# Optimization experiments

Hardware: AMD Instinct MI355X
Metric: run time of the kernel (lower is better)

## Reference

```python
import jax, jax.numpy as jnp
import numpy as np

B, C, H, W = 4, 256, 48, 48
HEADS, DIM_HEAD, SCALE = 8, 64, 10.0
INNER = HEADS * DIM_HEAD
EPS = 1e-12


def setup_inputs() -> dict:
    key = jax.random.key(0)
    k1, k2, k3, k4 = jax.random.split(key, 4)
    x = jax.random.normal(k1, (B, C, H, W), dtype=jnp.float32)
    # 1x1 conv weights stored as [out_ch, in_ch]
    w_qkv = jax.random.normal(k2, (3 * INNER, C), dtype=jnp.float32) * (1.0 / np.sqrt(C))
    w_out = jax.random.normal(k3, (C, INNER), dtype=jnp.float32) * (1.0 / np.sqrt(INNER))
    b_out = jax.random.normal(k4, (C,), dtype=jnp.float32) * 0.01
    return {"x": x, "w_qkv": w_qkv, "w_out": w_out, "b_out": b_out}


def _l2norm(t):
    # normalize along last axis, clamping the norm at EPS (matches torch l2norm)
    denom = jnp.maximum(jnp.linalg.norm(t, axis=-1, keepdims=True), EPS)
    return t / denom


def reference(x, w_qkv, w_out, b_out):
    b, c, h, w = x.shape
    n = h * w
    # 1x1 conv QKV projection: [B, 3*INNER, H, W]
    qkv = jnp.einsum('oc,bchw->bohw', w_qkv, x)
    q, k, v = jnp.split(qkv, 3, axis=1)
    # [B, heads, dim_head, N] -> [B, heads, N, dim_head]
    def to_bhnd(t):
        return t.reshape(b, HEADS, DIM_HEAD, n).transpose(0, 1, 3, 2)
    q = _l2norm(to_bhnd(q))
    k = _l2norm(to_bhnd(k))
    v = to_bhnd(v)
    sim = jnp.einsum('bhid,bhjd->bhij', q, k) * SCALE  # [B,h,N,N]
    attn = jax.nn.softmax(sim, axis=-1)
    out = jnp.einsum('bhij,bhjd->bhid', attn, v)  # [B,h,N,d]
    # back to [B, INNER, H, W]
    out = out.transpose(0, 1, 3, 2).reshape(b, INNER, h, w)
    # 1x1 conv output projection with bias
    out = jnp.einsum('oc,bchw->bohw', w_out, out) + b_out[None, :, None, None]
    return out
```

## Files before the change

### kernel.cpp

```cpp
#include <hip/hip_runtime.h>

typedef unsigned short u16;
typedef __attribute__((ext_vector_type(8))) short bf16x8;
typedef __attribute__((ext_vector_type(4))) float f32x4;
typedef __attribute__((ext_vector_type(16))) float f32x16;

#define MFMA16(A,B,C) __builtin_amdgcn_mfma_f32_16x16x32_bf16(A,B,C,0,0,0)
#define MFMA32(A,B,C) __builtin_amdgcn_mfma_f32_32x32x16_bf16(A,B,C,0,0,0)

#define B_ 4
#define C_ 256
#define N_ 2304
#define HEADS_ 8
#define DH_ 64
#define INNER_ 512
#define SCALE_LOG2E 14.426950408889634f

__device__ __forceinline__ u16 f2bf(float f) {
    union { float f; unsigned int u; } v; v.f = f;
    unsigned int r = v.u + 0x7fffu + ((v.u >> 16) & 1u);
    return (u16)(r >> 16);
}
__device__ __forceinline__ float bf2f(u16 h) {
    union { unsigned int u; float f; } v; v.u = ((unsigned int)h) << 16;
    return v.f;
}
__device__ __forceinline__ unsigned int cvtpk(float a, float b) {
    unsigned int r;
    asm("v_cvt_pk_bf16_f32 %0, %1, %2" : "=v"(r) : "v"(a), "v"(b));
    return r;
}
__device__ __forceinline__ void pl32swap(unsigned &a, unsigned &b) {
    asm volatile("v_permlane32_swap_b32 %0, %1" : "+v"(a), "+v"(b));
}
__device__ __forceinline__ float fexp2(float x) {
    float r;
    asm("v_exp_f32 %0, %1" : "=v"(r) : "v"(x));
    return r;
}

__global__ __launch_bounds__(256) void k_prep(const float* __restrict__ x,
                                              u16* __restrict__ xT,
                                              const float* __restrict__ w_qkv,
                                              u16* __restrict__ wqb,
                                              const float* __restrict__ w_out,
                                              u16* __restrict__ wob) {
    __shared__ float tile[64][65];
    int idx = blockIdx.x;
    int t = threadIdx.x;
    if (idx < 576) {
        int b = idx / 144, rem = idx % 144;
        int n0 = (rem >> 2) * 64, c0 = (rem & 3) * 64;
        const float* xb = x + (size_t)b * C_ * N_;
        u16* xTb = xT + (size_t)b * N_ * C_;
        int r = t >> 4;
        int q4 = (t & 15) * 4;
#pragma unroll
        for (int pass = 0; pass < 4; ++pass) {
            int c = r + pass * 16;
            float4 v = *(const float4*)(xb + (size_t)(c0 + c) * N_ + n0 + q4);
            tile[c][q4+0] = v.x; tile[c][q4+1] = v.y; tile[c][q4+2] = v.z; tile[c][q4+3] = v.w;
        }
        __syncthreads();
#pragma unroll
        for (int pass = 0; pass < 4; ++pass) {
            int n = r + pass * 16;
            ushort4 o;
            o.x = f2bf(tile[q4+0][n]); o.y = f2bf(tile[q4+1][n]);
            o.z = f2bf(tile[q4+2][n]); o.w = f2bf(tile[q4+3][n]);
            *(ushort4*)(xTb + (size_t)(n0 + n) * C_ + c0 + q4) = o;
        }
    } else if (idx < 960) {
        int i = (idx - 576) * 256 + t;
        float4 v = ((const float4*)w_qkv)[i];
        ushort4 o;
        o.x = f2bf(v.x); o.y = f2bf(v.y); o.z = f2bf(v.z); o.w = f2bf(v.w);
        ((ushort4*)wqb)[i] = o;
    } else {
        int i = (idx - 960) * 256 + t;
        float4 v = ((const float4*)w_out)[i];
        ushort4 o;
        o.x = f2bf(v.x); o.y = f2bf(v.y); o.z = f2bf(v.z); o.w = f2bf(v.w);
        ((ushort4*)wob)[i] = o;
    }
}

__global__ __launch_bounds__(256) void k_qkv(const u16* __restrict__ w_qkv,
                                             const u16* __restrict__ xT,
                                             u16* __restrict__ Qn,
                                             u16* __restrict__ Kn,
                                             u16* __restrict__ Vt) {
    __shared__ __align__(16) u16 Wt[64][264];
    __shared__ __align__(16) u16 Xt[64][264];
    int mt = blockIdx.x, nt = blockIdx.y, b = blockIdx.z;
    int tid = threadIdx.x;
    int wv = tid >> 6, lane = tid & 63;
    int col = lane & 15, quad = lane >> 4;
    int o0 = mt * 64;
    const u16* wtile = w_qkv + (size_t)o0 * C_;
    const u16* xtile = xT + ((size_t)b * N_ + nt*64) * C_;
#pragma unroll
    for (int p = 0; p < 8; ++p) {
        int c = p * 256 + tid;
        int row = c >> 5, seg = c & 31;
        *(uint4*)(&Wt[row][seg*8]) = *(const uint4*)(wtile + (size_t)row * C_ + seg*8);
        *(uint4*)(&Xt[row][seg*8]) = *(const uint4*)(xtile + (size_t)row * C_ + seg*8);
    }
    __syncthreads();
    f32x4 z = {0.f, 0.f, 0.f, 0.f};
    f32x4 acc[4]; acc[0]=z; acc[1]=z; acc[2]=z; acc[3]=z;
#pragma unroll
    for (int ks = 0; ks < 8; ++ks) {
        bf16x8 bfrag = *(const bf16x8*)(&Xt[wv*16 + col][ks*32 + quad*8]);
#pragma unroll
        for (int mb = 0; mb < 4; ++mb) {
            bf16x8 afrag = *(const bf16x8*)(&Wt[mb*16 + col][ks*32 + quad*8]);
            acc[mb] = MFMA16(afrag, bfrag, acc[mb]);
        }
    }
    int n = nt * 64 + wv * 16 + col;
    int which = mt >> 3, h = mt & 7;
    if (which < 2) {
        float s = 0.f;
#pragma unroll
        for (int mb = 0; mb < 4; ++mb)
#pragma unroll
            for (int r = 0; r < 4; ++r) s += acc[mb][r] * acc[mb][r];
        s += __shfl_xor(s, 16);
        s += __shfl_xor(s, 32);
        float inv = 1.f / fmaxf(sqrtf(s), 1e-12f);
        if (which == 0) inv *= SCALE_LOG2E;
        u16* dst = (which == 0 ? Qn : Kn) + (((size_t)b * HEADS_ + h) * N_ + n) * DH_;
#pragma unroll
        for (int mb = 0; mb < 4; ++mb) {
            uint2 o;
            o.x = cvtpk(acc[mb][0] * inv, acc[mb][1] * inv);
            o.y = cvtpk(acc[mb][2] * inv, acc[mb][3] * inv);
            *(uint2*)(dst + mb*16 + quad*4) = o;
        }
    } else {
        u16* dst = Vt + ((size_t)b * HEADS_ + h) * (size_t)DH_ * N_;
#pragma unroll
        for (int mb = 0; mb < 4; ++mb)
#pragma unroll
            for (int r = 0; r < 4; ++r)
                dst[(size_t)(mb*16 + quad*4 + r) * N_ + n] = f2bf(acc[mb][r]);
    }
}

__device__ __forceinline__ void store_o32(const f32x16 O, u16* dst, int hi) {
    unsigned c0 = cvtpk(O[0], O[1]),  c1 = cvtpk(O[2], O[3]);
    unsigned c2 = cvtpk(O[4], O[5]),  c3 = cvtpk(O[6], O[7]);
    unsigned c4 = cvtpk(O[8], O[9]),  c5 = cvtpk(O[10], O[11]);
    unsigned c6 = cvtpk(O[12], O[13]), c7 = cvtpk(O[14], O[15]);
    pl32swap(c0, c2); pl32swap(c1, c3);
    pl32swap(c4, c6); pl32swap(c5, c7);
    uint4 w0; w0.x = c0; w0.y = c1; w0.z = c2; w0.w = c3;
    uint4 w1; w1.x = c4; w1.y = c5; w1.z = c6; w1.w = c7;
    *(uint4*)(dst + hi*8)      = w0;
    *(uint4*)(dst + 16 + hi*8) = w1;
}

#define SM_PACK(S, PF0, PF1, LSUM)                                              \
    {                                                                           \
        _Pragma("unroll")                                                       \
        for (int i = 0; i < 16; ++i) S[i] = fexp2(S[i]);                        \
        LSUM += ( ((S[0]+S[1])+(S[2]+S[3])) + ((S[4]+S[5])+(S[6]+S[7])) )       \
              + ( ((S[8]+S[9])+(S[10]+S[11])) + ((S[12]+S[13])+(S[14]+S[15])) );\
        unsigned c0 = cvtpk(S[0], S[1]),  c1 = cvtpk(S[2], S[3]);               \
        unsigned c2 = cvtpk(S[4], S[5]),  c3 = cvtpk(S[6], S[7]);               \
        unsigned c4 = cvtpk(S[8], S[9]),  c5 = cvtpk(S[10], S[11]);             \
        unsigned c6 = cvtpk(S[12], S[13]), c7 = cvtpk(S[14], S[15]);            \
        pl32swap(c0, c2); pl32swap(c1, c3);                                     \
        pl32swap(c4, c6); pl32swap(c5, c7);                                     \
        PF0.u[0] = c0; PF0.u[1] = c1; PF0.u[2] = c2; PF0.u[3] = c3;             \
        PF1.u[0] = c4; PF1.u[1] = c5; PF1.u[2] = c6; PF1.u[3] = c7;             \
    }

__global__ __launch_bounds__(256) void k_attn_split(const u16* __restrict__ Qn,
                                                    const u16* __restrict__ Kn,
                                                    const u16* __restrict__ Vt,
                                                    u16* __restrict__ Opb,
                                                    float* __restrict__ lp) {
    __shared__ __align__(16) u16 Kt[2][64][72];
    __shared__ __align__(16) u16 Vtl[2][64][72];
    int head_lin = blockIdx.x & 31;
    int rest = blockIdx.x >> 5;
    int qt = rest % 18;
    int ksplit = rest / 18;
    int b = head_lin >> 3, h = head_lin & 7;
    int tid = threadIdx.x;
    int wv = tid >> 6, lane = tid & 63;
    int q32 = lane & 31, hi = lane >> 5;
    size_t head = (size_t)b * HEADS_ + h;
    const u16* Qh = Qn + head * (size_t)N_ * DH_;
    const u16* Kh = Kn + head * (size_t)N_ * DH_ + (size_t)ksplit * 576 * DH_;
    const u16* Vh = Vt + head * (size_t)DH_ * N_;
    int q0 = qt * 128 + wv * 32;
    bf16x8 qf[4];
#pragma unroll
    for (int ds = 0; ds < 4; ++ds)
        qf[ds] = *(const bf16x8*)(Qh + (size_t)(q0 + q32) * DH_ + ds*16 + hi*8);
    f32x16 accO0, accO1;
#pragma unroll
    for (int i = 0; i < 16; ++i) { accO0[i] = 0.f; accO1[i] = 0.f; }
    float lsum = 0.f;
    int srow = tid >> 3, sseg = tid & 7;
    const u16* ksrc0 = Kh + (size_t)tid * 8;
    const u16* vsrc0 = Vh + (size_t)srow * N_ + ksplit * 576 + sseg * 8;

    uint4 k0 = *(const uint4*)(ksrc0);
    uint4 k1 = *(const uint4*)(ksrc0 + 2048);
    uint4 v0 = *(const uint4*)(vsrc0);
    uint4 v1 = *(const uint4*)(vsrc0 + (size_t)32 * N_);
    *(uint4*)(&Kt[0][srow][sseg*8])       = k0;
    *(uint4*)(&Kt[0][32 + srow][sseg*8])  = k1;
    *(uint4*)(&Vtl[0][srow][sseg*8])      = v0;
    *(uint4*)(&Vtl[0][32 + srow][sseg*8]) = v1;
    int cur = 0;

    for (int kt = 0; kt < 9; ++kt) {
        __syncthreads();
        int ktn = kt + 1 < 9 ? kt + 1 : kt;
        k0 = *(const uint4*)(ksrc0 + (size_t)ktn * 4096);
        k1 = *(const uint4*)(ksrc0 + (size_t)ktn * 4096 + 2048);
        v0 = *(const uint4*)(vsrc0 + ktn * 64);
        v1 = *(const uint4*)(vsrc0 + (size_t)32 * N_ + ktn * 64);
        const u16 (*Ktc)[72]  = Kt[cur];
        const u16 (*Vtc)[72]  = Vtl[cur];
        f32x16 s0, s1;
#pragma unroll
        for (int i = 0; i < 16; ++i) { s0[i] = 0.f; s1[i] = 0.f; }
        __builtin_amdgcn_s_setprio(1);
#pragma unroll
        for (int ds = 0; ds < 4; ++ds) {
            bf16x8 kf = *(const bf16x8*)(&Ktc[q32][ds*16 + hi*8]);
            s0 = MFMA32(kf, qf[ds], s0);
        }
#pragma unroll
        for (int ds = 0; ds < 4; ++ds) {
            bf16x8 kf = *(const bf16x8*)(&Ktc[32 + q32][ds*16 + hi*8]);
            s1 = MFMA32(kf, qf[ds], s1);
        }
        __builtin_amdgcn_s_setprio(0);
        union { unsigned u[4]; bf16x8 v; } pfA, pfB, pfC, pfD;
        SM_PACK(s0, pfA, pfB, lsum)
        __builtin_amdgcn_s_setprio(1);
        {
            bf16x8 vf00 = *(const bf16x8*)(&Vtc[q32][hi*8]);
            bf16x8 vf01 = *(const bf16x8*)(&Vtc[32 + q32][hi*8]);
            accO0 = MFMA32(vf00, pfA.v, accO0);
            accO1 = MFMA32(vf01, pfA.v, accO1);
            bf16x8 vf10 = *(const bf16x8*)(&Vtc[q32][16 + hi*8]);
            bf16x8 vf11 = *(const bf16x8*)(&Vtc[32 + q32][16 + hi*8]);
            accO0 = MFMA32(vf10, pfB.v, accO0);
            accO1 = MFMA32(vf11, pfB.v, accO1);
        }
        __builtin_amdgcn_s_setprio(0);
        SM_PACK(s1, pfC, pfD, lsum)
        __builtin_amdgcn_s_setprio(1);
        {
            bf16x8 vf00 = *(const bf16x8*)(&Vtc[q32][32 + hi*8]);
            bf16x8 vf01 = *(const bf16x8*)(&Vtc[32 + q32][32 + hi*8]);
            accO0 = MFMA32(vf00, pfC.v, accO0);
            accO1 = MFMA32(vf01, pfC.v, accO1);
            bf16x8 vf10 = *(const bf16x8*)(&Vtc[q32][48 + hi*8]);
            bf16x8 vf11 = *(const bf16x8*)(&Vtc[32 + q32][48 + hi*8]);
            accO0 = MFMA32(vf10, pfD.v, accO0);
            accO1 = MFMA32(vf11, pfD.v, accO1);
        }
        __builtin_amdgcn_s_setprio(0);
        {
            u16 (*Ktn_)[72] = Kt[cur ^ 1];
            u16 (*Vtn_)[72] = Vtl[cur ^ 1];
            *(uint4*)(&Ktn_[srow][sseg*8])      = k0;
            *(uint4*)(&Ktn_[32 + srow][sseg*8]) = k1;
            *(uint4*)(&Vtn_[srow][sseg*8])      = v0;
            *(uint4*)(&Vtn_[32 + srow][sseg*8]) = v1;
        }
        cur ^= 1;
    }
    lsum += __shfl_xor(lsum, 32);
    u16* dst = Opb + (((size_t)ksplit * B_ + b) * N_ + q0 + q32) * INNER_ + h * DH_;
    store_o32(accO0, dst, hi);
    store_o32(accO1, dst + 32, hi);
    if (hi == 0) {
        size_t lbase = (((size_t)ksplit * B_ + b) * HEADS_ + h) * N_;
        lp[lbase + q0 + q32] = lsum;
    }
}

__global__ __launch_bounds__(256) void k_comb(const u16* __restrict__ Opb,
                                              const float* __restrict__ lp,
                                              u16* __restrict__ AO) {
    int g = blockIdx.x * 256 + threadIdx.x;
    int b = g / 294912;
    int rem = g % 294912;
    int n = rem >> 7;
    int i4 = rem & 127;
    int h = i4 >> 4;
    float s0 = 0.f, s1 = 0.f, s2 = 0.f, s3 = 0.f, l = 0.f;
#pragma unroll
    for (int s = 0; s < 4; ++s) {
        ushort4 p = ((const ushort4*)Opb)[g + (size_t)s * 1179648];
        s0 += bf2f(p.x); s1 += bf2f(p.y); s2 += bf2f(p.z); s3 += bf2f(p.w);
        l += lp[(((size_t)s * B_ + b) * HEADS_ + h) * N_ + n];
    }
    float inv = 1.f / l;
    uint2 o;
    o.x = cvtpk(s0 * inv, s1 * inv);
    o.y = cvtpk(s2 * inv, s3 * inv);
    ((uint2*)AO)[g] = o;
}

__global__ __launch_bounds__(256) void k_attn(const u16* __restrict__ Qn,
                                              const u16* __restrict__ Kn,
                                              const u16* __restrict__ Vt,
                                              u16* __restrict__ AO) {
    __shared__ __align__(16) u16 Kt[64][72];
    __shared__ __align__(16) u16 Vtl[64][72];
    __shared__ __align__(16) u16 plds[4][32][72];
    int head_lin = blockIdx.x & 31;
    int qt = blockIdx.x >> 5;
    int b = head_lin >> 3, h = head_lin & 7;
    int tid = threadIdx.x;
    int wv = tid >> 6, lane = tid & 63;
    int col = lane & 15, quad = lane >> 4;
    size_t head = (size_t)b * HEADS_ + h;
    const u16* Qh = Qn + head * (size_t)N_ * DH_;
    const u16* Kh = Kn + head * (size_t)N_ * DH_;
    const u16* Vh = Vt + head * (size_t)DH_ * N_;
    int q0 = qt * 128 + wv * 32;
    bf16x8 qfA0 = *(const bf16x8*)(Qh + (size_t)(q0 + col) * DH_ + quad*8);
    bf16x8 qfA1 = *(const bf16x8*)(Qh + (size_t)(q0 + col) * DH_ + 32 + quad*8);
    bf16x8 qfB0 = *(const bf16x8*)(Qh + (size_t)(q0 + 16 + col) * DH_ + quad*8);
    bf16x8 qfB1 = *(const bf16x8*)(Qh + (size_t)(q0 + 16 + col) * DH_ + 32 + quad*8);
    f32x4 z = {0.f, 0.f, 0.f, 0.f};
    f32x4 OA[4], OB[4];
#pragma unroll
    for (int i = 0; i < 4; ++i) { OA[i] = z; OB[i] = z; }
    float lA = 0.f, lB = 0.f;
    int srow = tid >> 3, sseg = tid & 7;
    const u16* ksrc0 = Kh + (size_t)tid * 8;
    const u16* vsrc0 = Vh + (size_t)srow * N_ + sseg * 8;
    uint4 k0 = *(const uint4*)(ksrc0);
    uint4 k1 = *(const uint4*)(ksrc0 + 2048);
    uint4 v0 = *(const uint4*)(vsrc0);
    uint4 v1 = *(const uint4*)(vsrc0 + (size_t)32 * N_);
    for (int kt = 0; kt < N_/64; ++kt) {
        *(uint4*)(&Kt[srow][sseg*8])      = k0;
        *(uint4*)(&Kt[32 + srow][sseg*8]) = k1;
        *(uint4*)(&Vtl[srow][sseg*8])      = v0;
        *(uint4*)(&Vtl[32 + srow][sseg*8]) = v1;
        __syncthreads();
        int ktn = kt + 1 < N_/64 ? kt + 1 : kt;
        k0 = *(const uint4*)(ksrc0 + (size_t)ktn * 4096);
        k1 = *(const uint4*)(ksrc0 + (size_t)ktn * 4096 + 2048);
        v0 = *(const uint4*)(vsrc0 + ktn * 64);
        v1 = *(const uint4*)(vsrc0 + (size_t)32 * N_ + ktn * 64);
        float rsA = 0.f, rsB = 0.f;
#pragma unroll
        for (int nb = 0; nb < 4; ++nb) {
            bf16x8 kf0 = *(const bf16x8*)(&Kt[nb*16 + col][quad*8]);
            bf16x8 kf1 = *(const bf16x8*)(&Kt[nb*16 + col][32 + quad*8]);
            f32x4 a = MFMA16(kf0, qfA0, z);
            a = MFMA16(kf1, qfA1, a);
            f32x4 c = MFMA16(kf0, qfB0, z);
            c = MFMA16(kf1, qfB1, c);
            float a0 = fexp2(a[0]);
            float a1 = fexp2(a[1]);
            float a2 = fexp2(a[2]);
            float a3 = fexp2(a[3]);
            float c0 = fexp2(c[0]);
            float c1 = fexp2(c[1]);
            float c2 = fexp2(c[2]);
            float c3 = fexp2(c[3]);
            rsA += (a0 + a1) + (a2 + a3);
            rsB += (c0 + c1) + (c2 + c3);
            uint2 wA, wB;
            wA.x = cvtpk(a0, a1); wA.y = cvtpk(a2, a3);
            wB.x = cvtpk(c0, c1); wB.y = cvtpk(c2, c3);
            *(uint2*)(&plds[wv][col][nb*16 + quad*4]) = wA;
            *(uint2*)(&plds[wv][16 + col][nb*16 + quad*4]) = wB;
        }
        lA += rsA; lB += rsB;
        __asm__ volatile("" ::: "memory");
#pragma unroll
        for (int ks = 0; ks < 2; ++ks) {
            bf16x8 pfA = *(const bf16x8*)(&plds[wv][col][ks*32 + quad*8]);
            bf16x8 pfB = *(const bf16x8*)(&plds[wv][16 + col][ks*32 + quad*8]);
#pragma unroll
            for (int nb = 0; nb < 4; ++nb) {
                bf16x8 vf = *(const bf16x8*)(&Vtl[nb*16 + col][ks*32 + quad*8]);
                OA[nb] = MFMA16(vf, pfA, OA[nb]);
                OB[nb] = MFMA16(vf, pfB, OB[nb]);
            }
        }
        __asm__ volatile("" ::: "memory");
        __syncthreads();
    }
    lA += __shfl_xor(lA, 16); lA += __shfl_xor(lA, 32);
    lB += __shfl_xor(lB, 16); lB += __shfl_xor(lB, 32);
    float linvA = 1.f / lA, linvB = 1.f / lB;
    u16* dstA = AO + ((size_t)b * N_ + q0 + col) * INNER_ + h * DH_;
    u16* dstB = AO + ((size_t)b * N_ + q0 + 16 + col) * INNER_ + h * DH_;
#pragma unroll
    for (int nb = 0; nb < 4; ++nb) {
        uint2 wA, wB;
        wA.x = cvtpk(OA[nb][0] * linvA, OA[nb][1] * linvA);
        wA.y = cvtpk(OA[nb][2] * linvA, OA[nb][3] * linvA);
        wB.x = cvtpk(OB[nb][0] * linvB, OB[nb][1] * linvB);
        wB.y = cvtpk(OB[nb][2] * linvB, OB[nb][3] * linvB);
        *(uint2*)(dstA + nb*16 + quad*4) = wA;
        *(uint2*)(dstB + nb*16 + quad*4) = wB;
    }
}

__global__ __launch_bounds__(256) void k_proj(const u16* __restrict__ w_out,
                                              const float* __restrict__ b_out,
                                              const u16* __restrict__ AO,
                                              float* __restrict__ out) {
    __shared__ __align__(16) u16 Wt[64][264];
    __shared__ __align__(16) u16 At[64][264];
    int mt = blockIdx.x, nt = blockIdx.y, b = blockIdx.z;
    int tid = threadIdx.x;
    int wv = tid >> 6, lane = tid & 63;
    int col = lane & 15, quad = lane >> 4;
    int o0b = mt * 64;
    const u16* wtile = w_out + (size_t)o0b * INNER_;
    const u16* atile = AO + ((size_t)b * N_ + nt*64) * INNER_;
    f32x4 z = {0.f, 0.f, 0.f, 0.f};
    f32x4 acc[4]; acc[0]=z; acc[1]=z; acc[2]=z; acc[3]=z;
#pragma unroll
    for (int half = 0; half < 2; ++half) {
        if (half) __syncthreads();
#pragma unroll
        for (int p = 0; p < 8; ++p) {
            int c = p * 256 + tid;
            int row = c >> 5, seg = c & 31;
            *(uint4*)(&Wt[row][seg*8]) =
                *(const uint4*)(wtile + (size_t)row * INNER_ + half*256 + seg*8);
            *(uint4*)(&At[row][seg*8]) =
                *(const uint4*)(atile + (size_t)row * INNER_ + half*256 + seg*8);
        }
        __syncthreads();
#pragma unroll
        for (int ks = 0; ks < 8; ++ks) {
            bf16x8 af = *(const bf16x8*)(&Wt[wv*16 + col][ks*32 + quad*8]);
#pragma unroll
            for (int nb = 0; nb < 4; ++nb) {
                bf16x8 bfv = *(const bf16x8*)(&At[nb*16 + col][ks*32 + quad*8]);
                acc[nb] = MFMA16(af, bfv, acc[nb]);
            }
        }
    }
    int o0 = o0b + wv * 16;
    float bias[4];
#pragma unroll
    for (int r = 0; r < 4; ++r) bias[r] = b_out[o0 + quad*4 + r];
    float* dst = out + ((size_t)b * C_ + o0) * N_ + nt*64;
#pragma unroll
    for (int nb = 0; nb < 4; ++nb)
#pragma unroll
        for (int r = 0; r < 4; ++r)
            dst[(size_t)(quad*4 + r) * N_ + nb*16 + col] = acc[nb][r] + bias[r];
}

extern "C" void kernel_launch(void* const* d_in, const int* in_sizes, int n_in,
                              void* d_out, int out_size, void* d_ws, size_t ws_size,
                              hipStream_t stream) {
    const float* x     = (const float*)d_in[0];
    const float* w_qkv = (const float*)d_in[1];
    const float* w_out = (const float*)d_in[2];
    const float* b_out = (const float*)d_in[3];
    float* out = (float*)d_out;

    char* ws = (char*)d_ws;
    u16* xT  = (u16*)(ws);
    u16* Qn  = (u16*)(ws + 4718592);
    u16* Kn  = (u16*)(ws + 14155776);
    u16* Vt  = (u16*)(ws + 23592960);
    u16* AO  = (u16*)(ws + 33030144);
    u16* wqb = (u16*)(ws + 42467328);
    u16* wob = (u16*)(ws + 43253760);
    u16* Opb = (u16*)(ws + 43515904);
    float* lp = (float*)(ws + 1179648);
    const size_t need = 81854464;

    hipLaunchKernelGGL(k_prep, dim3(1088), dim3(256), 0, stream, x, xT, w_qkv, wqb, w_out, wob);
    hipLaunchKernelGGL(k_qkv,  dim3(24, N_/64, B_), dim3(256), 0, stream, wqb, xT, Qn, Kn, Vt);
    if (ws_size >= need) {
        hipLaunchKernelGGL(k_attn_split, dim3(2304), dim3(256), 0, stream, Qn, Kn, Vt, Opb, lp);
        hipLaunchKernelGGL(k_comb, dim3(4608), dim3(256), 0, stream, Opb, lp, AO);
    } else {
        hipLaunchKernelGGL(k_attn, dim3((N_/128) * 32), dim3(256), 0, stream, Qn, Kn, Vt, AO);
    }
    hipLaunchKernelGGL(k_proj, dim3(C_/64, N_/64, B_), dim3(256), 0, stream, wob, b_out, AO, out);
}
```

Measured before the change: 167.0 us.

## Replace split-K attention and combine pass with 64-query single-pass attention blocks

Removes the four-way key split and the separate combine kernel. Each 128-thread block now handles 64 queries over the full key range and normalizes its output directly into AO. This drops the partial-output write and read traffic and one kernel launch. In exchange, each block runs a longer serial loop of 36 key tiles, and the grid has fewer, smaller blocks (1152 blocks of 128 threads instead of 2304 of 256), which can lower occupancy and latency hiding.

```diff
diff --git a/kernel.cpp b/kernel.cpp
--- a/kernel.cpp
+++ b/kernel.cpp
@@ -20,10 +20,6 @@
     union { float f; unsigned int u; } v; v.f = f;
     unsigned int r = v.u + 0x7fffu + ((v.u >> 16) & 1u);
     return (u16)(r >> 16);
-}
-__device__ __forceinline__ float bf2f(u16 h) {
-    union { unsigned int u; float f; } v; v.u = ((unsigned int)h) << 16;
-    return v.f;
 }
 __device__ __forceinline__ unsigned int cvtpk(float a, float b) {
     unsigned int r;
@@ -148,11 +144,11 @@
     }
 }
 
-__device__ __forceinline__ void store_o32(const f32x16 O, u16* dst, int hi) {
-    unsigned c0 = cvtpk(O[0], O[1]),  c1 = cvtpk(O[2], O[3]);
-    unsigned c2 = cvtpk(O[4], O[5]),  c3 = cvtpk(O[6], O[7]);
-    unsigned c4 = cvtpk(O[8], O[9]),  c5 = cvtpk(O[10], O[11]);
-    unsigned c6 = cvtpk(O[12], O[13]), c7 = cvtpk(O[14], O[15]);
+__device__ __forceinline__ void store_o32n(const f32x16 O, float inv, u16* dst, int hi) {
+    unsigned c0 = cvtpk(O[0]*inv,  O[1]*inv),  c1 = cvtpk(O[2]*inv,  O[3]*inv);
+    unsigned c2 = cvtpk(O[4]*inv,  O[5]*inv),  c3 = cvtpk(O[6]*inv,  O[7]*inv);
+    unsigned c4 = cvtpk(O[8]*inv,  O[9]*inv),  c5 = cvtpk(O[10]*inv, O[11]*inv);
+    unsigned c6 = cvtpk(O[12]*inv, O[13]*inv), c7 = cvtpk(O[14]*inv, O[15]*inv);
     pl32swap(c0, c2); pl32swap(c1, c3);
     pl32swap(c4, c6); pl32swap(c5, c7);
     uint4 w0; w0.x = c0; w0.y = c1; w0.z = c2; w0.w = c3;
@@ -177,26 +173,23 @@
         PF1.u[0] = c4; PF1.u[1] = c5; PF1.u[2] = c6; PF1.u[3] = c7;             \
     }
 
-__global__ __launch_bounds__(256) void k_attn_split(const u16* __restrict__ Qn,
-                                                    const u16* __restrict__ Kn,
-                                                    const u16* __restrict__ Vt,
-                                                    u16* __restrict__ Opb,
-                                                    float* __restrict__ lp) {
+__global__ __launch_bounds__(128) void k_attn64(const u16* __restrict__ Qn,
+                                                const u16* __restrict__ Kn,
+                                                const u16* __restrict__ Vt,
+                                                u16* __restrict__ AO) {
     __shared__ __align__(16) u16 Kt[2][64][72];
     __shared__ __align__(16) u16 Vtl[2][64][72];
     int head_lin = blockIdx.x & 31;
-    int rest = blockIdx.x >> 5;
-    int qt = rest % 18;
-    int ksplit = rest / 18;
+    int qt = blockIdx.x >> 5;
     int b = head_lin >> 3, h = head_lin & 7;
     int tid = threadIdx.x;
     int wv = tid >> 6, lane = tid & 63;
     int q32 = lane & 31, hi = lane >> 5;
     size_t head = (size_t)b * HEADS_ + h;
     const u16* Qh = Qn + head * (size_t)N_ * DH_;
-    const u16* Kh = Kn + head * (size_t)N_ * DH_ + (size_t)ksplit * 576 * DH_;
+    const u16* Kh = Kn + head * (size_t)N_ * DH_;
     const u16* Vh = Vt + head * (size_t)DH_ * N_;
-    int q0 = qt * 128 + wv * 32;
+    int q0 = qt * 64 + wv * 32;
     bf16x8 qf[4];
 #pragma unroll
     for (int ds = 0; ds < 4; ++ds)
@@ -207,25 +200,37 @@
     float lsum = 0.f;
     int srow = tid >> 3, sseg = tid & 7;
     const u16* ksrc0 = Kh + (size_t)tid * 8;
-    const u16* vsrc0 = Vh + (size_t)srow * N_ + ksplit * 576 + sseg * 8;
+    const u16* vsrc0 = Vh + (size_t)srow * N_ + sseg * 8;
 
     uint4 k0 = *(const uint4*)(ksrc0);
-    uint4 k1 = *(const uint4*)(ksrc0 + 2048);
+    uint4 k1 = *(const uint4*)(ksrc0 + 1024);
+    uint4 k2 = *(const uint4*)(ksrc0 + 2048);
+    uint4 k3 = *(const uint4*)(ksrc0 + 3072);
     uint4 v0 = *(const uint4*)(vsrc0);
-    uint4 v1 = *(const uint4*)(vsrc0 + (size_t)32 * N_);
+    uint4 v1 = *(const uint4*)(vsrc0 + (size_t)16 * N_);
+    uint4 v2 = *(const uint4*)(vsrc0 + (size_t)32 * N_);
+    uint4 v3 = *(const uint4*)(vsrc0 + (size_t)48 * N_);
     *(uint4*)(&Kt[0][srow][sseg*8])       = k0;
-    *(uint4*)(&Kt[0][32 + srow][sseg*8])  = k1;
+    *(uint4*)(&Kt[0][16 + srow][sseg*8])  = k1;
+    *(uint4*)(&Kt[0][32 + srow][sseg*8])  = k2;
+    *(uint4*)(&Kt[0][48 + srow][sseg*8])  = k3;
     *(uint4*)(&Vtl[0][srow][sseg*8])      = v0;
-    *(uint4*)(&Vtl[0][32 + srow][sseg*8]) = v1;
+    *(uint4*)(&Vtl[0][16 + srow][sseg*8]) = v1;
+    *(uint4*)(&Vtl[0][32 + srow][sseg*8]) = v2;
+    *(uint4*)(&Vtl[0][48 + srow][sseg*8]) = v3;
     int cur = 0;
 
-    for (int kt = 0; kt < 9; ++kt) {
+    for (int kt = 0; kt < 36; ++kt) {
         __syncthreads();
-        int ktn = kt + 1 < 9 ? kt + 1 : kt;
+        int ktn = kt + 1 < 36 ? kt + 1 : kt;
         k0 = *(const uint4*)(ksrc0 + (size_t)ktn * 4096);
-        k1 = *(const uint4*)(ksrc0 + (size_t)ktn * 4096 + 2048);
+        k1 = *(const uint4*)(ksrc0 + (size_t)ktn * 4096 + 1024);
+        k2 = *(const uint4*)(ksrc0 + (size_t)ktn * 4096 + 2048);
+        k3 = *(const uint4*)(ksrc0 + (size_t)ktn * 4096 + 3072);
         v0 = *(const uint4*)(vsrc0 + ktn * 64);
-        v1 = *(const uint4*)(vsrc0 + (size_t)32 * N_ + ktn * 64);
+        v1 = *(const uint4*)(vsrc0 + (size_t)16 * N_ + ktn * 64);
+        v2 = *(const uint4*)(vsrc0 + (size_t)32 * N_ + ktn * 64);
+        v3 = *(const uint4*)(vsrc0 + (size_t)48 * N_ + ktn * 64);
         const u16 (*Ktc)[72]  = Kt[cur];
         const u16 (*Vtc)[72]  = Vtl[cur];
         f32x16 s0, s1;
@@ -274,146 +279,21 @@
             u16 (*Ktn_)[72] = Kt[cur ^ 1];
             u16 (*Vtn_)[72] = Vtl[cur ^ 1];
             *(uint4*)(&Ktn_[srow][sseg*8])      = k0;
-            *(uint4*)(&Ktn_[32 + srow][sseg*8]) = k1;
+            *(uint4*)(&Ktn_[16 + srow][sseg*8]) = k1;
+            *(uint4*)(&Ktn_[32 + srow][sseg*8]) = k2;
+            *(uint4*)(&Ktn_[48 + srow][sseg*8]) = k3;
             *(uint4*)(&Vtn_[srow][sseg*8])      = v0;
-            *(uint4*)(&Vtn_[32 + srow][sseg*8]) = v1;
+            *(uint4*)(&Vtn_[16 + srow][sseg*8]) = v1;
+            *(uint4*)(&Vtn_[32 + srow][sseg*8]) = v2;
+            *(uint4*)(&Vtn_[48 + srow][sseg*8]) = v3;
         }
         cur ^= 1;
     }
     lsum += __shfl_xor(lsum, 32);
-    u16* dst = Opb + (((size_t)ksplit * B_ + b) * N_ + q0 + q32) * INNER_ + h * DH_;
-    store_o32(accO0, dst, hi);
-    store_o32(accO1, dst + 32, hi);
-    if (hi == 0) {
-        size_t lbase = (((size_t)ksplit * B_ + b) * HEADS_ + h) * N_;
-        lp[lbase + q0 + q32] = lsum;
-    }
-}
-
-__global__ __launch_bounds__(256) void k_comb(const u16* __restrict__ Opb,
-                                              const float* __restrict__ lp,
-                                              u16* __restrict__ AO) {
-    int g = blockIdx.x * 256 + threadIdx.x;
-    int b = g / 294912;
-    int rem = g % 294912;
-    int n = rem >> 7;
-    int i4 = rem & 127;
-    int h = i4 >> 4;
-    float s0 = 0.f, s1 = 0.f, s2 = 0.f, s3 = 0.f, l = 0.f;
-#pragma unroll
-    for (int s = 0; s < 4; ++s) {
-        ushort4 p = ((const ushort4*)Opb)[g + (size_t)s * 1179648];
-        s0 += bf2f(p.x); s1 += bf2f(p.y); s2 += bf2f(p.z); s3 += bf2f(p.w);
-        l += lp[(((size_t)s * B_ + b) * HEADS_ + h) * N_ + n];
-    }
-    float inv = 1.f / l;
-    uint2 o;
-    o.x = cvtpk(s0 * inv, s1 * inv);
-    o.y = cvtpk(s2 * inv, s3 * inv);
-    ((uint2*)AO)[g] = o;
-}
-
-__global__ __launch_bounds__(256) void k_attn(const u16* __restrict__ Qn,
-                                              const u16* __restrict__ Kn,
-                                              const u16* __restrict__ Vt,
-                                              u16* __restrict__ AO) {
-    __shared__ __align__(16) u16 Kt[64][72];
-    __shared__ __align__(16) u16 Vtl[64][72];
-    __shared__ __align__(16) u16 plds[4][32][72];
-    int head_lin = blockIdx.x & 31;
-    int qt = blockIdx.x >> 5;
-    int b = head_lin >> 3, h = head_lin & 7;
-    int tid = threadIdx.x;
-    int wv = tid >> 6, lane = tid & 63;
-    int col = lane & 15, quad = lane >> 4;
-    size_t head = (size_t)b * HEADS_ + h;
-    const u16* Qh = Qn + head * (size_t)N_ * DH_;
-    const u16* Kh = Kn + head * (size_t)N_ * DH_;
-    const u16* Vh = Vt + head * (size_t)DH_ * N_;
-    int q0 = qt * 128 + wv * 32;
-    bf16x8 qfA0 = *(const bf16x8*)(Qh + (size_t)(q0 + col) * DH_ + quad*8);
-    bf16x8 qfA1 = *(const bf16x8*)(Qh + (size_t)(q0 + col) * DH_ + 32 + quad*8);
-    bf16x8 qfB0 = *(const bf16x8*)(Qh + (size_t)(q0 + 16 + col) * DH_ + quad*8);
-    bf16x8 qfB1 = *(const bf16x8*)(Qh + (size_t)(q0 + 16 + col) * DH_ + 32 + quad*8);
-    f32x4 z = {0.f, 0.f, 0.f, 0.f};
-    f32x4 OA[4], OB[4];
-#pragma unroll
-    for (int i = 0; i < 4; ++i) { OA[i] = z; OB[i] = z; }
-    float lA = 0.f, lB = 0.f;
-    int srow = tid >> 3, sseg = tid & 7;
-    const u16* ksrc0 = Kh + (size_t)tid * 8;
-    const u16* vsrc0 = Vh + (size_t)srow * N_ + sseg * 8;
-    uint4 k0 = *(const uint4*)(ksrc0);
-    uint4 k1 = *(const uint4*)(ksrc0 + 2048);
-    uint4 v0 = *(const uint4*)(vsrc0);
-    uint4 v1 = *(const uint4*)(vsrc0 + (size_t)32 * N_);
-    for (int kt = 0; kt < N_/64; ++kt) {
-        *(uint4*)(&Kt[srow][sseg*8])      = k0;
-        *(uint4*)(&Kt[32 + srow][sseg*8]) = k1;
-        *(uint4*)(&Vtl[srow][sseg*8])      = v0;
-        *(uint4*)(&Vtl[32 + srow][sseg*8]) = v1;
-        __syncthreads();
-        int ktn = kt + 1 < N_/64 ? kt + 1 : kt;
-        k0 = *(const uint4*)(ksrc0 + (size_t)ktn * 4096);
-        k1 = *(const uint4*)(ksrc0 + (size_t)ktn * 4096 + 2048);
-        v0 = *(const uint4*)(vsrc0 + ktn * 64);
-        v1 = *(const uint4*)(vsrc0 + (size_t)32 * N_ + ktn * 64);
-        float rsA = 0.f, rsB = 0.f;
-#pragma unroll
-        for (int nb = 0; nb < 4; ++nb) {
-            bf16x8 kf0 = *(const bf16x8*)(&Kt[nb*16 + col][quad*8]);
-            bf16x8 kf1 = *(const bf16x8*)(&Kt[nb*16 + col][32 + quad*8]);
-            f32x4 a = MFMA16(kf0, qfA0, z);
-            a = MFMA16(kf1, qfA1, a);
-            f32x4 c = MFMA16(kf0, qfB0, z);
-            c = MFMA16(kf1, qfB1, c);
-            float a0 = fexp2(a[0]);
-            float a1 = fexp2(a[1]);
-            float a2 = fexp2(a[2]);
-            float a3 = fexp2(a[3]);
-            float c0 = fexp2(c[0]);
-            float c1 = fexp2(c[1]);
-            float c2 = fexp2(c[2]);
-            float c3 = fexp2(c[3]);
-            rsA += (a0 + a1) + (a2 + a3);
-            rsB += (c0 + c1) + (c2 + c3);
-            uint2 wA, wB;
-            wA.x = cvtpk(a0, a1); wA.y = cvtpk(a2, a3);
-            wB.x = cvtpk(c0, c1); wB.y = cvtpk(c2, c3);
-            *(uint2*)(&plds[wv][col][nb*16 + quad*4]) = wA;
-            *(uint2*)(&plds[wv][16 + col][nb*16 + quad*4]) = wB;
-        }
-        lA += rsA; lB += rsB;
-        __asm__ volatile("" ::: "memory");
-#pragma unroll
-        for (int ks = 0; ks < 2; ++ks) {
-            bf16x8 pfA = *(const bf16x8*)(&plds[wv][col][ks*32 + quad*8]);
-            bf16x8 pfB = *(const bf16x8*)(&plds[wv][16 + col][ks*32 + quad*8]);
-#pragma unroll
-            for (int nb = 0; nb < 4; ++nb) {
-                bf16x8 vf = *(const bf16x8*)(&Vtl[nb*16 + col][ks*32 + quad*8]);
-                OA[nb] = MFMA16(vf, pfA, OA[nb]);
-                OB[nb] = MFMA16(vf, pfB, OB[nb]);
-            }
-        }
-        __asm__ volatile("" ::: "memory");
-        __syncthreads();
-    }
-    lA += __shfl_xor(lA, 16); lA += __shfl_xor(lA, 32);
-    lB += __shfl_xor(lB, 16); lB += __shfl_xor(lB, 32);
-    float linvA = 1.f / lA, linvB = 1.f / lB;
-    u16* dstA = AO + ((size_t)b * N_ + q0 + col) * INNER_ + h * DH_;
-    u16* dstB = AO + ((size_t)b * N_ + q0 + 16 + col) * INNER_ + h * DH_;
-#pragma unroll
-    for (int nb = 0; nb < 4; ++nb) {
-        uint2 wA, wB;
-        wA.x = cvtpk(OA[nb][0] * linvA, OA[nb][1] * linvA);
-        wA.y = cvtpk(OA[nb][2] * linvA, OA[nb][3] * linvA);
-        wB.x = cvtpk(OB[nb][0] * linvB, OB[nb][1] * linvB);
-        wB.y = cvtpk(OB[nb][2] * linvB, OB[nb][3] * linvB);
-        *(uint2*)(dstA + nb*16 + quad*4) = wA;
-        *(uint2*)(dstB + nb*16 + quad*4) = wB;
-    }
+    float inv = 1.f / lsum;
+    u16* dst = AO + ((size_t)b * N_ + q0 + q32) * INNER_ + h * DH_;
+    store_o32n(accO0, inv, dst, hi);
+    store_o32n(accO1, inv, dst + 32, hi);
 }
 
 __global__ __launch_bounds__(256) void k_proj(const u16* __restrict__ w_out,
@@ -483,17 +363,9 @@
     u16* AO  = (u16*)(ws + 33030144);
     u16* wqb = (u16*)(ws + 42467328);
     u16* wob = (u16*)(ws + 43253760);
-    u16* Opb = (u16*)(ws + 43515904);
-    float* lp = (float*)(ws + 1179648);
-    const size_t need = 81854464;
 
     hipLaunchKernelGGL(k_prep, dim3(1088), dim3(256), 0, stream, x, xT, w_qkv, wqb, w_out, wob);
     hipLaunchKernelGGL(k_qkv,  dim3(24, N_/64, B_), dim3(256), 0, stream, wqb, xT, Qn, Kn, Vt);
-    if (ws_size >= need) {
-        hipLaunchKernelGGL(k_attn_split, dim3(2304), dim3(256), 0, stream, Qn, Kn, Vt, Opb, lp);
-        hipLaunchKernelGGL(k_comb, dim3(4608), dim3(256), 0, stream, Opb, lp, AO);
-    } else {
-        hipLaunchKernelGGL(k_attn, dim3((N_/128) * 32), dim3(256), 0, stream, Qn, Kn, Vt, AO);
-    }
+    hipLaunchKernelGGL(k_attn64, dim3(1152), dim3(128), 0, stream, Qn, Kn, Vt, AO);
     hipLaunchKernelGGL(k_proj, dim3(C_/64, N_/64, B_), dim3(256), 0, stream, wob, b_out, AO, out);
 }
```

Result: slower. 178.6 us (+6.9%).

## Fuse split-K attention combine into output projection and streamline attention inner loop

Applied to the files above, without the earlier changes.

Removes the separate combine kernel. The four split-K partial outputs and their row sums are now reduced and normalised while the output-projection kernel loads its activation tile, which saves one launch and a write/read round trip of the combined activations. In exchange, each projection block (C/64=4 blocks per tile) reads all four partials, so partial reads are duplicated across output-channel tiles. The attention loop also switches to pointer-increment addressing and zero-initialised MFMA accumulators to trim address arithmetic.

```diff
diff --git a/kernel.cpp b/kernel.cpp
--- a/kernel.cpp
+++ b/kernel.cpp
@@ -37,6 +37,11 @@
     float r;
     asm("v_exp_f32 %0, %1" : "=v"(r) : "v"(x));
     return r;
+}
+__device__ __forceinline__ void bfacc(unsigned u, float &lo, float &hi) {
+    union { unsigned x; float f; } a, c;
+    a.x = u << 16; c.x = u & 0xffff0000u;
+    lo += a.f; hi += c.f;
 }
 
 __global__ __launch_bounds__(256) void k_prep(const float* __restrict__ x,
@@ -201,9 +206,12 @@
 #pragma unroll
     for (int ds = 0; ds < 4; ++ds)
         qf[ds] = *(const bf16x8*)(Qh + (size_t)(q0 + q32) * DH_ + ds*16 + hi*8);
-    f32x16 accO0, accO1;
-#pragma unroll
-    for (int i = 0; i < 16; ++i) { accO0[i] = 0.f; accO1[i] = 0.f; }
+    float z0 = 0.f;
+    asm volatile("" : "+v"(z0));
+    f32x16 zv;
+#pragma unroll
+    for (int i = 0; i < 16; ++i) zv[i] = z0;
+    f32x16 accO0 = zv, accO1 = zv;
     float lsum = 0.f;
     int srow = tid >> 3, sseg = tid & 7;
     const u16* ksrc0 = Kh + (size_t)tid * 8;
@@ -217,58 +225,46 @@
     *(uint4*)(&Kt[0][32 + srow][sseg*8])  = k1;
     *(uint4*)(&Vtl[0][srow][sseg*8])      = v0;
     *(uint4*)(&Vtl[0][32 + srow][sseg*8]) = v1;
+    const u16* kp = ksrc0 + 4096;
+    const u16* vp = vsrc0 + 64;
     int cur = 0;
 
     for (int kt = 0; kt < 9; ++kt) {
         __syncthreads();
-        int ktn = kt + 1 < 9 ? kt + 1 : kt;
-        k0 = *(const uint4*)(ksrc0 + (size_t)ktn * 4096);
-        k1 = *(const uint4*)(ksrc0 + (size_t)ktn * 4096 + 2048);
-        v0 = *(const uint4*)(vsrc0 + ktn * 64);
-        v1 = *(const uint4*)(vsrc0 + (size_t)32 * N_ + ktn * 64);
-        const u16 (*Ktc)[72]  = Kt[cur];
-        const u16 (*Vtc)[72]  = Vtl[cur];
+        k0 = *(const uint4*)(kp);
+        k1 = *(const uint4*)(kp + 2048);
+        v0 = *(const uint4*)(vp);
+        v1 = *(const uint4*)(vp + (size_t)32 * N_);
+        kp += 4096; vp += 64;
+        const u16* kb0 = &Kt[cur][q32][hi*8];
+        const u16* kb1 = kb0 + 32*72;
+        const u16* vb0 = &Vtl[cur][q32][hi*8];
+        const u16* vb1 = vb0 + 32*72;
         f32x16 s0, s1;
-#pragma unroll
-        for (int i = 0; i < 16; ++i) { s0[i] = 0.f; s1[i] = 0.f; }
         __builtin_amdgcn_s_setprio(1);
-#pragma unroll
-        for (int ds = 0; ds < 4; ++ds) {
-            bf16x8 kf = *(const bf16x8*)(&Ktc[q32][ds*16 + hi*8]);
-            s0 = MFMA32(kf, qf[ds], s0);
-        }
-#pragma unroll
-        for (int ds = 0; ds < 4; ++ds) {
-            bf16x8 kf = *(const bf16x8*)(&Ktc[32 + q32][ds*16 + hi*8]);
-            s1 = MFMA32(kf, qf[ds], s1);
-        }
+        s0 = MFMA32(*(const bf16x8*)(kb0),      qf[0], zv);
+        s0 = MFMA32(*(const bf16x8*)(kb0 + 16), qf[1], s0);
+        s0 = MFMA32(*(const bf16x8*)(kb0 + 32), qf[2], s0);
+        s0 = MFMA32(*(const bf16x8*)(kb0 + 48), qf[3], s0);
+        s1 = MFMA32(*(const bf16x8*)(kb1),      qf[0], zv);
+        s1 = MFMA32(*(const bf16x8*)(kb1 + 16), qf[1], s1);
+        s1 = MFMA32(*(const bf16x8*)(kb1 + 32), qf[2], s1);
+        s1 = MFMA32(*(const bf16x8*)(kb1 + 48), qf[3], s1);
         __builtin_amdgcn_s_setprio(0);
         union { unsigned u[4]; bf16x8 v; } pfA, pfB, pfC, pfD;
         SM_PACK(s0, pfA, pfB, lsum)
         __builtin_amdgcn_s_setprio(1);
-        {
-            bf16x8 vf00 = *(const bf16x8*)(&Vtc[q32][hi*8]);
-            bf16x8 vf01 = *(const bf16x8*)(&Vtc[32 + q32][hi*8]);
-            accO0 = MFMA32(vf00, pfA.v, accO0);
-            accO1 = MFMA32(vf01, pfA.v, accO1);
-            bf16x8 vf10 = *(const bf16x8*)(&Vtc[q32][16 + hi*8]);
-            bf16x8 vf11 = *(const bf16x8*)(&Vtc[32 + q32][16 + hi*8]);
-            accO0 = MFMA32(vf10, pfB.v, accO0);
-            accO1 = MFMA32(vf11, pfB.v, accO1);
-        }
+        accO0 = MFMA32(*(const bf16x8*)(vb0),      pfA.v, accO0);
+        accO1 = MFMA32(*(const bf16x8*)(vb1),      pfA.v, accO1);
+        accO0 = MFMA32(*(const bf16x8*)(vb0 + 16), pfB.v, accO0);
+        accO1 = MFMA32(*(const bf16x8*)(vb1 + 16), pfB.v, accO1);
         __builtin_amdgcn_s_setprio(0);
         SM_PACK(s1, pfC, pfD, lsum)
         __builtin_amdgcn_s_setprio(1);
-        {
-            bf16x8 vf00 = *(const bf16x8*)(&Vtc[q32][32 + hi*8]);
-            bf16x8 vf01 = *(const bf16x8*)(&Vtc[32 + q32][32 + hi*8]);
-            accO0 = MFMA32(vf00, pfC.v, accO0);
-            accO1 = MFMA32(vf01, pfC.v, accO1);
-            bf16x8 vf10 = *(const bf16x8*)(&Vtc[q32][48 + hi*8]);
-            bf16x8 vf11 = *(const bf16x8*)(&Vtc[32 + q32][48 + hi*8]);
-            accO0 = MFMA32(vf10, pfD.v, accO0);
-            accO1 = MFMA32(vf11, pfD.v, accO1);
-        }
+        accO0 = MFMA32(*(const bf16x8*)(vb0 + 32), pfC.v, accO0);
+        accO1 = MFMA32(*(const bf16x8*)(vb1 + 32), pfC.v, accO1);
+        accO0 = MFMA32(*(const bf16x8*)(vb0 + 48), pfD.v, accO0);
+        accO1 = MFMA32(*(const bf16x8*)(vb1 + 48), pfD.v, accO1);
         __builtin_amdgcn_s_setprio(0);
         {
             u16 (*Ktn_)[72] = Kt[cur ^ 1];
@@ -288,29 +284,6 @@
         size_t lbase = (((size_t)ksplit * B_ + b) * HEADS_ + h) * N_;
         lp[lbase + q0 + q32] = lsum;
     }
-}
-
-__global__ __launch_bounds__(256) void k_comb(const u16* __restrict__ Opb,
-                                              const float* __restrict__ lp,
-                                              u16* __restrict__ AO) {
-    int g = blockIdx.x * 256 + threadIdx.x;
-    int b = g / 294912;
-    int rem = g % 294912;
-    int n = rem >> 7;
-    int i4 = rem & 127;
-    int h = i4 >> 4;
-    float s0 = 0.f, s1 = 0.f, s2 = 0.f, s3 = 0.f, l = 0.f;
-#pragma unroll
-    for (int s = 0; s < 4; ++s) {
-        ushort4 p = ((const ushort4*)Opb)[g + (size_t)s * 1179648];
-        s0 += bf2f(p.x); s1 += bf2f(p.y); s2 += bf2f(p.z); s3 += bf2f(p.w);
-        l += lp[(((size_t)s * B_ + b) * HEADS_ + h) * N_ + n];
-    }
-    float inv = 1.f / l;
-    uint2 o;
-    o.x = cvtpk(s0 * inv, s1 * inv);
-    o.y = cvtpk(s2 * inv, s3 * inv);
-    ((uint2*)AO)[g] = o;
 }
 
 __global__ __launch_bounds__(256) void k_attn(const u16* __restrict__ Qn,
@@ -416,6 +389,83 @@
     }
 }
 
+__global__ __launch_bounds__(256) void k_projc(const u16* __restrict__ w_out,
+                                               const float* __restrict__ b_out,
+                                               const u16* __restrict__ Opb,
+                                               const float* __restrict__ lp,
+                                               float* __restrict__ out) {
+    __shared__ __align__(16) u16 Wt[64][264];
+    __shared__ __align__(16) u16 At[64][264];
+    __shared__ float invl[8][64];
+    int mt = blockIdx.x, nt = blockIdx.y, b = blockIdx.z;
+    int tid = threadIdx.x;
+    int wv = tid >> 6, lane = tid & 63;
+    int col = lane & 15, quad = lane >> 4;
+#pragma unroll
+    for (int e = tid; e < 512; e += 256) {
+        int hh = e >> 6, nr = e & 63;
+        int n = nt * 64 + nr;
+        float l = 0.f;
+#pragma unroll
+        for (int s = 0; s < 4; ++s)
+            l += lp[(((size_t)s * B_ + b) * HEADS_ + hh) * N_ + n];
+        invl[hh][nr] = 1.f / l;
+    }
+    __syncthreads();
+    int o0b = mt * 64;
+    const u16* wtile = w_out + (size_t)o0b * INNER_;
+    const size_t arow = (size_t)b * N_ + nt * 64;
+    f32x4 z = {0.f, 0.f, 0.f, 0.f};
+    f32x4 acc[4]; acc[0]=z; acc[1]=z; acc[2]=z; acc[3]=z;
+#pragma unroll
+    for (int half = 0; half < 2; ++half) {
+        if (half) __syncthreads();
+#pragma unroll
+        for (int p = 0; p < 8; ++p) {
+            int c = p * 256 + tid;
+            int row = c >> 5, seg = c & 31;
+            *(uint4*)(&Wt[row][seg*8]) =
+                *(const uint4*)(wtile + (size_t)row * INNER_ + half*256 + seg*8);
+            int ic = half*256 + seg*8;
+            size_t g = (arow + row) * INNER_ + ic;
+            uint4 p0 = *(const uint4*)(Opb + g);
+            uint4 p1 = *(const uint4*)(Opb + g + 4718592);
+            uint4 p2 = *(const uint4*)(Opb + g + 2*4718592);
+            uint4 p3 = *(const uint4*)(Opb + g + 3*4718592);
+            float s0=0.f,s1=0.f,s2=0.f,s3=0.f,s4=0.f,s5=0.f,s6=0.f,s7=0.f;
+            bfacc(p0.x,s0,s1); bfacc(p0.y,s2,s3); bfacc(p0.z,s4,s5); bfacc(p0.w,s6,s7);
+            bfacc(p1.x,s0,s1); bfacc(p1.y,s2,s3); bfacc(p1.z,s4,s5); bfacc(p1.w,s6,s7);
+            bfacc(p2.x,s0,s1); bfacc(p2.y,s2,s3); bfacc(p2.z,s4,s5); bfacc(p2.w,s6,s7);
+            bfacc(p3.x,s0,s1); bfacc(p3.y,s2,s3); bfacc(p3.z,s4,s5); bfacc(p3.w,s6,s7);
+            float inv = invl[ic >> 6][row];
+            uint4 o;
+            o.x = cvtpk(s0*inv, s1*inv); o.y = cvtpk(s2*inv, s3*inv);
+            o.z = cvtpk(s4*inv, s5*inv); o.w = cvtpk(s6*inv, s7*inv);
+            *(uint4*)(&At[row][seg*8]) = o;
+        }
+        __syncthreads();
+#pragma unroll
+        for (int ks = 0; ks < 8; ++ks) {
+            bf16x8 af = *(const bf16x8*)(&Wt[wv*16 + col][ks*32 + quad*8]);
+#pragma unroll
+            for (int nb = 0; nb < 4; ++nb) {
+                bf16x8 bfv = *(const bf16x8*)(&At[nb*16 + col][ks*32 + quad*8]);
+                acc[nb] = MFMA16(af, bfv, acc[nb]);
+            }
+        }
+    }
+    int o0 = o0b + wv * 16;
+    float bias[4];
+#pragma unroll
+    for (int r = 0; r < 4; ++r) bias[r] = b_out[o0 + quad*4 + r];
+    float* dst = out + ((size_t)b * C_ + o0) * N_ + nt*64;
+#pragma unroll
+    for (int nb = 0; nb < 4; ++nb)
+#pragma unroll
+        for (int r = 0; r < 4; ++r)
+            dst[(size_t)(quad*4 + r) * N_ + nb*16 + col] = acc[nb][r] + bias[r];
+}
+
 __global__ __launch_bounds__(256) void k_proj(const u16* __restrict__ w_out,
                                               const float* __restrict__ b_out,
                                               const u16* __restrict__ AO,
@@ -491,9 +541,9 @@
     hipLaunchKernelGGL(k_qkv,  dim3(24, N_/64, B_), dim3(256), 0, stream, wqb, xT, Qn, Kn, Vt);
     if (ws_size >= need) {
         hipLaunchKernelGGL(k_attn_split, dim3(2304), dim3(256), 0, stream, Qn, Kn, Vt, Opb, lp);
-        hipLaunchKernelGGL(k_comb, dim3(4608), dim3(256), 0, stream, Opb, lp, AO);
+        hipLaunchKernelGGL(k_projc, dim3(C_/64, N_/64, B_), dim3(256), 0, stream, wob, b_out, Opb, lp, out);
     } else {
         hipLaunchKernelGGL(k_attn, dim3((N_/128) * 32), dim3(256), 0, stream, Qn, Kn, Vt, AO);
-    }
-    hipLaunchKernelGGL(k_proj, dim3(C_/64, N_/64, B_), dim3(256), 0, stream, wob, b_out, AO, out);
-}
+        hipLaunchKernelGGL(k_proj, dim3(C_/64, N_/64, B_), dim3(256), 0, stream, wob, b_out, AO, out);
+    }
+}
```

New measurement: 173.7 us. +4.0%, slower.
